# Optimization experiments

Measured on AMD Instinct MI355X. Metric: run time of the kernel, lower is better.

The kernel has to match this reference:

```python
import jax, jax.numpy as jnp
import numpy as np

D_WIN = 6
SIGMA = D_WIN / 2.0  # sigma = D/2
EPS = 1e-6


def _ln(x, g, b):
    m = jnp.mean(x, -1, keepdims=True)
    v = jnp.var(x, -1, keepdims=True)
    return (x - m) / jnp.sqrt(v + EPS) * g + b


def _cross_attn(q, kv, Wq, Wkv, Wproj, bproj, nh):
    # standard multi-head cross attention, no qkv bias (qkv_bias=False)
    B, S, C = q.shape
    N = kv.shape[1]
    hd = C // nh
    scale = hd ** -0.5
    qh = (q @ Wq).reshape(B, S, nh, hd).transpose(0, 2, 1, 3) * scale
    kvh = (kv @ Wkv).reshape(B, N, 2, nh, hd).transpose(2, 0, 3, 1, 4)
    k, v = kvh[0], kvh[1]
    attn = jax.nn.softmax(jnp.einsum('bhsd,bhnd->bhsn', qh, k), -1)
    x = jnp.einsum('bhsn,bhnd->bhsd', attn, v).transpose(0, 2, 1, 3).reshape(B, S, C)
    return x @ Wproj + bproj


def setup_inputs() -> dict:
    key = jax.random.key(0)
    ks = jax.random.split(key, 32)
    B, S, C, H, W = 32, 128, 384, 8, 512

    def lin(k, i, o):
        return jax.random.normal(k, (i, o), jnp.float32) * 0.02

    inp = {
        'q': jax.random.normal(ks[0], (B, S, C), jnp.float32),
        'kv': jax.random.normal(ks[1], (B, H * W, C), jnp.float32),
        # main attention linears (qkv_bias=False)
        'Wq': lin(ks[2], C, C),
        'Wkv': lin(ks[3], C, 2 * C),
        'Wproj': lin(ks[4], C, C), 'bproj': jnp.zeros((C,), jnp.float32),
        # position predictor
        'Wp_w': lin(ks[5], C, C), 'Wp_b': jnp.zeros((C,), jnp.float32),
        'vp_w': lin(ks[6], C, 1), 'vp_b': jnp.zeros((1,), jnp.float32),
        'Wqpos': lin(ks[7], C, C), 'bqpos': jnp.zeros((C,), jnp.float32),
        # simplified RCTC decoder projection
        'Wrctc': lin(ks[8], C, C), 'brctc': jnp.zeros((C,), jnp.float32),
        # pt_to_question cross attention (2 heads)
        'ca1_Wq': lin(ks[9], C, C), 'ca1_Wkv': lin(ks[10], C, 2 * C),
        'ca1_Wproj': lin(ks[11], C, C), 'ca1_bproj': jnp.zeros((C,), jnp.float32),
        # pt_to_image cross attention (2 heads)
        'ca2_Wq': lin(ks[12], C, C), 'ca2_Wkv': lin(ks[13], C, 2 * C),
        'ca2_Wproj': lin(ks[14], C, C), 'ca2_bproj': jnp.zeros((C,), jnp.float32),
        # layernorms
        'g_q1': jnp.ones((C,), jnp.float32), 'b_q1': jnp.zeros((C,), jnp.float32),
        'g_kv1': jnp.ones((C,), jnp.float32), 'b_kv1': jnp.zeros((C,), jnp.float32),
        'g_q2': jnp.ones((C,), jnp.float32), 'b_q2': jnp.zeros((C,), jnp.float32),
        'g_kv2': jnp.ones((C,), jnp.float32), 'b_kv2': jnp.zeros((C,), jnp.float32),
        'sz_h': H, 'sz_w': W,
    }
    return inp


def reference(q, kv, Wq, Wkv, Wproj, bproj, Wp_w, Wp_b, vp_w, vp_b, Wqpos, bqpos,
              Wrctc, brctc, ca1_Wq, ca1_Wkv, ca1_Wproj, ca1_bproj,
              ca2_Wq, ca2_Wkv, ca2_Wproj, ca2_bproj,
              g_q1, b_q1, g_kv1, b_kv1, g_q2, b_q2, g_kv2, b_kv2, sz_h, sz_w):
    B, N, C = kv.shape
    S = q.shape[1]
    H, W = sz_h, sz_w
    nh = 1
    hd = C // nh
    scale = hd ** -0.5

    # RCTC decoder (simplified): (B,N,C) -> (B,C,H,W) -> collapse H -> (B,W,C) -> linear
    kv_img = kv.transpose(0, 2, 1).reshape(B, C, H, W)
    dec = kv_img.mean(axis=2).transpose(0, 2, 1)  # (B, W, C)
    dec = dec @ Wrctc + brctc

    qh = (q @ Wq).reshape(B, S, nh, hd).transpose(0, 2, 1, 3) * scale  # (B,nh,S,hd)
    kvh = (dec @ Wkv).reshape(B, W, 2, nh, hd).transpose(2, 0, 3, 1, 4)
    k, v = kvh[0], kvh[1]  # (B,nh,W,hd)

    # position prediction branch
    p = q @ Wqpos + bqpos
    p = _cross_attn(_ln(p, g_q1, b_q1), _ln(q, g_kv1, b_kv1),
                    ca1_Wq, ca1_Wkv, ca1_Wproj, ca1_bproj, 2)
    p = _cross_attn(_ln(p, g_q2, b_q2), _ln(dec, g_kv2, b_kv2),
                    ca2_Wq, ca2_Wkv, ca2_Wproj, ca2_bproj, 2)
    p_t = jax.nn.sigmoid(jnp.tanh(p @ Wp_w + Wp_b) @ vp_w + vp_b) * W  # (B,S,1)

    # Gaussian window mask around predicted position
    idx = jnp.arange(W, dtype=jnp.float32)[None, None, None, :]     # (1,1,1,W)
    pexp = p_t[:, None, :, :]                                        # (B,1,S,1)
    gauss = jnp.exp(-(idx - pexp) ** 2 / (2.0 * SIGMA ** 2))         # (B,1,S,W)

    attn = jnp.einsum('bhsd,bhwd->bhsw', qh, k) * gauss
    attn = jax.nn.softmax(attn, -1)
    x = jnp.einsum('bhsw,bhwd->bhsd', attn, v).transpose(0, 2, 1, 3).reshape(B, S, C)
    return x @ Wproj + bproj
```

## Files before the change

kernel.cpp:

```cpp
#include <hip/hip_runtime.h>
#include <hip/hip_bf16.h>
#include <math.h>

#define B_ 32
#define S_ 128
#define C_ 384
#define H_ 8
#define W_ 512
#define NKV 4096

typedef __attribute__((ext_vector_type(8))) short short8;
typedef __attribute__((ext_vector_type(4))) float floatx4;

static __device__ __forceinline__ ushort f2bf(float v) {
    __hip_bfloat16 h = __float2bfloat16(v);
    return *(ushort*)&h;
}
static __device__ __forceinline__ float ldf(const float* p, size_t i) { return p[i]; }
static __device__ __forceinline__ float ldf(const ushort* p, size_t i) {
    union { uint u; float f; } c; c.u = (uint)p[i] << 16; return c.f;
}

static __device__ __forceinline__ void gl_lds16(const ushort* g, ushort* l) {
    __builtin_amdgcn_global_load_lds(
        (const __attribute__((address_space(1))) void*)g,
        (__attribute__((address_space(3))) void*)l, 16, 0, 0);
}

__global__ __launch_bounds__(256) void mean_kernel(const float* __restrict__ kv,
                                                   ushort* __restrict__ dec0b) {
    int v = blockIdx.x * blockDim.x + threadIdx.x;
    int total = B_ * W_ * (C_ / 4);
    if (v >= total) return;
    int c4  = v % (C_ / 4);
    int row = v / (C_ / 4);
    int b = row / W_;
    int w = row % W_;
    const float4* src = (const float4*)kv + (size_t)(b * NKV + w) * (C_ / 4) + c4;
    float4 s = {0.f, 0.f, 0.f, 0.f};
#pragma unroll
    for (int h = 0; h < H_; ++h) {
        float4 t = src[(size_t)h * W_ * (C_ / 4)];
        s.x += t.x; s.y += t.y; s.z += t.z; s.w += t.w;
    }
    ushort4 o;
    o.x = f2bf(s.x * 0.125f); o.y = f2bf(s.y * 0.125f);
    o.z = f2bf(s.z * 0.125f); o.w = f2bf(s.w * 0.125f);
    ((ushort4*)dec0b)[v] = o;
}

__global__ __launch_bounds__(256) void cast_kernel(const float* __restrict__ in,
                                                   ushort* __restrict__ out, int n4) {
    int v = blockIdx.x * blockDim.x + threadIdx.x;
    if (v >= n4) return;
    float4 f = ((const float4*)in)[v];
    ushort4 o;
    o.x = f2bf(f.x); o.y = f2bf(f.y); o.z = f2bf(f.z); o.w = f2bf(f.w);
    ((ushort4*)out)[v] = o;
}

struct WtDesc { const float* src[12]; ushort* dst[12]; int Kd[12]; int Nd[12]; };
__global__ __launch_bounds__(256) void wtcast_kernel(WtDesc d) {
    int wi = blockIdx.y;
    int idx = blockIdx.x * 256 + threadIdx.x;
    int K = d.Kd[wi], N = d.Nd[wi];
    if (idx >= K * N) return;
    int n = idx / K, k = idx % K;
    d.dst[wi][idx] = f2bf(d.src[wi][(size_t)k * N + n]);
}

__global__ __launch_bounds__(256) void bgemm_kernel(
    const ushort* __restrict__ A, const ushort* __restrict__ Bt,
    const float* __restrict__ bias, float* __restrict__ Cout,
    ushort* __restrict__ Cbf, int M, int N, int K, float alpha, int act)
{
    __shared__ ushort As[128 * 32];
    __shared__ ushort Bs[128 * 32];
    const int tid = threadIdx.x;
    const int bm = blockIdx.y * 128, bn = blockIdx.x * 128;
    const int wav = tid >> 6, lane = tid & 63;
    const int wm = (wav >> 1) * 64, wn = (wav & 1) * 64;
    const int lrow = lane & 15, lq = lane >> 4;

    floatx4 acc[4][4] = {};

    const int crow = tid >> 2, ccol = (tid & 3) * 8;
    const ushort* Ag0 = A + (size_t)(bm + crow) * K + ccol;
    const ushort* Ag1 = Ag0 + (size_t)64 * K;
    const ushort* Bg0 = Bt + (size_t)(bn + crow) * K + ccol;
    const ushort* Bg1 = Bg0 + (size_t)64 * K;
    ushort* AsP0 = &As[tid * 8];
    ushort* AsP1 = &As[2048 + tid * 8];
    ushort* BsP0 = &Bs[tid * 8];
    ushort* BsP1 = &Bs[2048 + tid * 8];

    for (int k0 = 0; k0 < K; k0 += 32) {
        gl_lds16(Ag0 + k0, AsP0);
        gl_lds16(Ag1 + k0, AsP1);
        gl_lds16(Bg0 + k0, BsP0);
        gl_lds16(Bg1 + k0, BsP1);
        __syncthreads();
        short8 af[4], bfr[4];
#pragma unroll
        for (int i = 0; i < 4; ++i)
            af[i] = *(const short8*)&As[(wm + 16 * i + lrow) * 32 + lq * 8];
#pragma unroll
        for (int j = 0; j < 4; ++j)
            bfr[j] = *(const short8*)&Bs[(wn + 16 * j + lrow) * 32 + lq * 8];
#pragma unroll
        for (int i = 0; i < 4; ++i)
#pragma unroll
            for (int j = 0; j < 4; ++j)
                acc[i][j] = __builtin_amdgcn_mfma_f32_16x16x32_bf16(af[i], bfr[j], acc[i][j], 0, 0, 0);
        __syncthreads();
    }

#pragma unroll
    for (int i = 0; i < 4; ++i)
#pragma unroll
        for (int j = 0; j < 4; ++j) {
            int row = bm + wm + 16 * i + lq * 4;
            int col = bn + wn + 16 * j + lrow;
            float bv = bias ? bias[col] : 0.f;
#pragma unroll
            for (int r = 0; r < 4; ++r) {
                float v = acc[i][j][r] * alpha + bv;
                if (act == 1) v = tanhf(v);
                size_t off = (size_t)(row + r) * N + col;
                if (Cout) Cout[off] = v;
                if (Cbf) Cbf[off] = f2bf(v);
            }
        }
}

static inline void bgemm(hipStream_t st, const ushort* A, const ushort* Bt,
                         const float* bias, float* Cout, ushort* Cbf,
                         int M, int N, int K, float alpha, int act) {
    dim3 grid(N / 128, M / 128), block(256);
    bgemm_kernel<<<grid, block, 0, st>>>(A, Bt, bias, Cout, Cbf, M, N, K, alpha, act);
}

struct BGArgs {
    const ushort* A; const ushort* Bt;
    const float* bias; float* outF; ushort* outB;
    int lda, ldb, ldo;
    long AsB, BsB, OsB;
    int AsH, BsH, OsH;
    int K, NH;
    float alpha; int act;
};
__global__ __launch_bounds__(256) void battn_kernel(BGArgs g) {
    __shared__ ushort As[128 * 40];
    __shared__ ushort Bs[64 * 40];
    const int bn = blockIdx.x * 64, bm = blockIdx.y * 128;
    const int bat = blockIdx.z, bb = bat / g.NH, hh = bat % g.NH;
    const ushort* A  = g.A  + (size_t)bb * g.AsB + (size_t)hh * g.AsH;
    const ushort* Bt = g.Bt + (size_t)bb * g.BsB + (size_t)hh * g.BsH;
    const int tid = threadIdx.x;
    const int wav = tid >> 6, lane = tid & 63;
    const int lrow = lane & 15, lq = lane >> 4;
    const int sr = tid >> 2, sc0 = (tid & 3) * 8;
    const ushort* Ag0 = A + (size_t)(bm + sr) * g.lda + sc0;
    const ushort* Ag1 = A + (size_t)(bm + sr + 64) * g.lda + sc0;
    const ushort* Bg  = Bt + (size_t)(bn + sr) * g.ldb + sc0;
    ushort* Asw0 = &As[sr * 40 + sc0];
    ushort* Asw1 = &As[(sr + 64) * 40 + sc0];
    ushort* Bsw  = &Bs[sr * 40 + sc0];

    floatx4 acc[2][4] = {};

    for (int k0 = 0; k0 < g.K; k0 += 32) {
        uint4 a0 = *(const uint4*)(Ag0 + k0);
        uint4 a1 = *(const uint4*)(Ag1 + k0);
        uint4 b  = *(const uint4*)(Bg + k0);
        __syncthreads();
        *(uint4*)Asw0 = a0; *(uint4*)Asw1 = a1; *(uint4*)Bsw = b;
        __syncthreads();
        short8 af0 = *(const short8*)&As[(wav * 32 + lrow) * 40 + lq * 8];
        short8 af1 = *(const short8*)&As[(wav * 32 + 16 + lrow) * 40 + lq * 8];
#pragma unroll
        for (int j = 0; j < 4; ++j) {
            short8 bf = *(const short8*)&Bs[(16 * j + lrow) * 40 + lq * 8];
            acc[0][j] = __builtin_amdgcn_mfma_f32_16x16x32_bf16(af0, bf, acc[0][j], 0, 0, 0);
            acc[1][j] = __builtin_amdgcn_mfma_f32_16x16x32_bf16(af1, bf, acc[1][j], 0, 0, 0);
        }
    }

#pragma unroll
    for (int i = 0; i < 2; ++i)
#pragma unroll
        for (int j = 0; j < 4; ++j) {
            int col = bn + 16 * j + lrow;
            float bv = g.bias ? g.bias[col] : 0.f;
            int row0 = bm + wav * 32 + 16 * i + lq * 4;
#pragma unroll
            for (int r = 0; r < 4; ++r) {
                float v = acc[i][j][r] * g.alpha + bv;
                if (g.act == 1) v = tanhf(v);
                size_t off = (size_t)bb * g.OsB + (size_t)hh * g.OsH
                           + (size_t)(row0 + r) * g.ldo + col;
                if (g.outF) g.outF[off] = v;
                if (g.outB) g.outB[off] = f2bf(v);
            }
        }
}

static inline void battn(hipStream_t st, const ushort* A, const ushort* Bt,
                         const float* bias, float* outF, ushort* outB,
                         int M, int N, int K, float alpha, int act,
                         int lda, long AsB, int AsH,
                         int ldb, long BsB, int BsH,
                         int ldo, long OsB, int OsH,
                         int NH, int nbat) {
    BGArgs g;
    g.A = A; g.Bt = Bt; g.bias = bias; g.outF = outF; g.outB = outB;
    g.lda = lda; g.ldb = ldb; g.ldo = ldo;
    g.AsB = AsB; g.BsB = BsB; g.OsB = OsB;
    g.AsH = AsH; g.BsH = BsH; g.OsH = OsH;
    g.K = K; g.NH = NH; g.alpha = alpha; g.act = act;
    dim3 grid(N / 64, M / 128, nbat);
    battn_kernel<<<grid, 256, 0, st>>>(g);
}

static inline void bgemm64(hipStream_t st, const ushort* A, const ushort* Bt,
                           const float* bias, float* outF, ushort* outB,
                           int M, int N, int K, float alpha, int act) {
    battn(st, A, Bt, bias, outF, outB, M, N, K, alpha, act,
          K, 0, 0, K, 0, 0, N, 0, 0, 1, 1);
}

template <typename T>
__global__ __launch_bounds__(128) void ln_kernel(const T* __restrict__ X,
    const float* __restrict__ g, const float* __restrict__ bb,
    ushort* __restrict__ Y) {
    int row = blockIdx.x;
    const T* x = X + (size_t)row * C_;
    ushort* y = Y + (size_t)row * C_;
    int t = threadIdx.x;
    float v0 = ldf(x, t), v1 = ldf(x, t + 128), v2 = ldf(x, t + 256);
    float s = v0 + v1 + v2, sq = v0 * v0 + v1 * v1 + v2 * v2;
    __shared__ float rs[128], rq[128];
    rs[t] = s; rq[t] = sq; __syncthreads();
    if (t < 64) {
        s = rs[t] + rs[t + 64]; sq = rq[t] + rq[t + 64];
        for (int o = 32; o; o >>= 1) { s += __shfl_down(s, o); sq += __shfl_down(sq, o); }
        if (t == 0) { rs[0] = s; rq[0] = sq; }
    }
    __syncthreads();
    float mean = rs[0] * (1.0f / C_);
    float var  = rq[0] * (1.0f / C_) - mean * mean;
    float inv  = rsqrtf(var + 1e-6f);
    y[t]       = f2bf((v0 - mean) * inv * g[t]       + bb[t]);
    y[t + 128] = f2bf((v1 - mean) * inv * g[t + 128] + bb[t + 128]);
    y[t + 256] = f2bf((v2 - mean) * inv * g[t + 256] + bb[t + 256]);
}

template <int NW, int GAUSS>
__global__ __launch_bounds__(256) void softmax_kernel(
    const float* __restrict__ sc, const float* __restrict__ ptv,
    ushort* __restrict__ P)
{
    int row = blockIdx.x * 4 + (threadIdx.x >> 6);
    int lane = threadIdx.x & 63;
    const float* s = sc + (size_t)row * NW;
    float pcen = GAUSS ? ptv[row] : 0.f;
    float vals[NW / 64];
    float m = -1e30f;
#pragma unroll
    for (int i = 0; i < NW / 64; ++i) {
        int w = lane + 64 * i;
        float v = s[w];
        if (GAUSS) { float dw = (float)w - pcen; v *= expf(dw * dw * (-1.0f / 18.0f)); }
        vals[i] = v; m = fmaxf(m, v);
    }
#pragma unroll
    for (int o = 32; o; o >>= 1) m = fmaxf(m, __shfl_xor(m, o));
    float sum = 0.f;
#pragma unroll
    for (int i = 0; i < NW / 64; ++i) { vals[i] = expf(vals[i] - m); sum += vals[i]; }
#pragma unroll
    for (int o = 32; o; o >>= 1) sum += __shfl_xor(sum, o);
    float rinv = 1.0f / sum;
    ushort* op = P + (size_t)row * NW;
#pragma unroll
    for (int i = 0; i < NW / 64; ++i) op[lane + 64 * i] = f2bf(vals[i] * rinv);
}

__global__ __launch_bounds__(256) void vtrans_kernel(
    const ushort* __restrict__ kvb, ushort* __restrict__ vt,
    int Nw, int C2, int CC)
{
    int b = blockIdx.z;
    int w0 = blockIdx.x * 32, c0 = blockIdx.y * 32;
    __shared__ ushort t[32][33];
    int tid = threadIdx.x;
    int wl = tid >> 3, c4 = (tid & 7) * 4;
    ushort4 v = *(const ushort4*)&kvb[((size_t)b * Nw + w0 + wl) * C2 + CC + c0 + c4];
    t[wl][c4] = v.x; t[wl][c4 + 1] = v.y; t[wl][c4 + 2] = v.z; t[wl][c4 + 3] = v.w;
    __syncthreads();
    int dl = tid >> 3, w4 = (tid & 7) * 4;
    ushort4 o;
    o.x = t[w4][dl]; o.y = t[w4 + 1][dl]; o.z = t[w4 + 2][dl]; o.w = t[w4 + 3][dl];
    *(ushort4*)&vt[((size_t)b * CC + c0 + dl) * Nw + w0 + w4] = o;
}

__global__ __launch_bounds__(128) void pt_kernel(const float* __restrict__ T,
    const float* __restrict__ vpw, const float* __restrict__ vpb,
    float* __restrict__ out) {
    int row = blockIdx.x;
    int t = threadIdx.x;
    const float* x = T + (size_t)row * C_;
    float s = x[t] * vpw[t] + x[t + 128] * vpw[t + 128] + x[t + 256] * vpw[t + 256];
    __shared__ float red[128];
    red[t] = s; __syncthreads();
    if (t < 64) {
        s = red[t] + red[t + 64];
        for (int o = 32; o; o >>= 1) s += __shfl_down(s, o);
        if (t == 0) {
            float z = s + vpb[0];
            out[row] = 512.0f / (1.0f + expf(-z));
        }
    }
}

extern "C" void kernel_launch(void* const* d_in, const int* in_sizes, int n_in,
                              void* d_out, int out_size, void* d_ws, size_t ws_size,
                              hipStream_t stream) {
    const float* q     = (const float*)d_in[0];
    const float* kv    = (const float*)d_in[1];
    const float* Wq    = (const float*)d_in[2];
    const float* Wkv   = (const float*)d_in[3];
    const float* Wproj = (const float*)d_in[4];
    const float* bproj = (const float*)d_in[5];
    const float* Wp_w  = (const float*)d_in[6];
    const float* Wp_b  = (const float*)d_in[7];
    const float* vp_w  = (const float*)d_in[8];
    const float* vp_b  = (const float*)d_in[9];
    const float* Wqpos = (const float*)d_in[10];
    const float* bqpos = (const float*)d_in[11];
    const float* Wrctc = (const float*)d_in[12];
    const float* brctc = (const float*)d_in[13];
    const float* ca1_Wq    = (const float*)d_in[14];
    const float* ca1_Wkv   = (const float*)d_in[15];
    const float* ca1_Wproj = (const float*)d_in[16];
    const float* ca1_bproj = (const float*)d_in[17];
    const float* ca2_Wq    = (const float*)d_in[18];
    const float* ca2_Wkv   = (const float*)d_in[19];
    const float* ca2_Wproj = (const float*)d_in[20];
    const float* ca2_bproj = (const float*)d_in[21];
    const float* g_q1  = (const float*)d_in[22];
    const float* b_q1  = (const float*)d_in[23];
    const float* g_kv1 = (const float*)d_in[24];
    const float* b_kv1 = (const float*)d_in[25];
    const float* g_q2  = (const float*)d_in[26];
    const float* b_q2  = (const float*)d_in[27];
    const float* g_kv2 = (const float*)d_in[28];
    const float* b_kv2 = (const float*)d_in[29];
    float* out = (float*)d_out;
    float* ws  = (float*)d_ws;

    ushort* dec0b = (ushort*)(ws);
    ushort* wb    = (ushort*)(ws + 3145728);
    ushort* qb    = (ushort*)(ws + 4251648);
    ushort* decb  = (ushort*)(ws + 5038080);
    ushort* qhb   = (ushort*)(ws + 8183808);
    float*  p     = ws + 8970240;
    ushort* pb    = (ushort*)(ws + 10543104);
    float*  t1    = ws + 11329536;
    ushort* t1b   = (ushort*)(ws + 12902400);
    ushort* t2b   = (ushort*)(ws + 13688832);
    ushort* qpb   = (ushort*)(ws + 16834560);
    ushort* kvb   = (ushort*)(ws + 17620992);
    ushort* vt    = (ushort*)(ws + 23912448);
    float*  sc    = ws + 27058176;
    ushort* Pb    = (ushort*)(ws + 31252480);
    ushort* xb    = (ushort*)(ws + 33349632);
    float*  ptb   = ws + 34136064;

    ushort* wbWq     = wb;
    ushort* wbWqpos  = wb + 147456;
    ushort* wbWrctc  = wb + 294912;
    ushort* wbC1Wq   = wb + 442368;
    ushort* wbC1Wp   = wb + 589824;
    ushort* wbC2Wq   = wb + 737280;
    ushort* wbC2Wp   = wb + 884736;
    ushort* wbWpw    = wb + 1032192;
    ushort* wbWproj  = wb + 1179648;
    ushort* wbWkv    = wb + 1327104;
    ushort* wbC1Wkv  = wb + 1622016;
    ushort* wbC2Wkv  = wb + 1916928;

    const float rs384 = 0.05103103630798288f;
    const float rs192 = 0.07216878364870323f;

    mean_kernel<<<(B_ * W_ * (C_ / 4) + 255) / 256, 256, 0, stream>>>(kv, dec0b);
    {
        WtDesc d;
        const float* s_[12] = {Wq, Wqpos, Wrctc, ca1_Wq, ca1_Wproj, ca2_Wq, ca2_Wproj,
                               Wp_w, Wproj, Wkv, ca1_Wkv, ca2_Wkv};
        ushort* t_[12] = {wbWq, wbWqpos, wbWrctc, wbC1Wq, wbC1Wp, wbC2Wq, wbC2Wp,
                          wbWpw, wbWproj, wbWkv, wbC1Wkv, wbC2Wkv};
        for (int i = 0; i < 12; ++i) {
            d.src[i] = s_[i]; d.dst[i] = t_[i];
            d.Kd[i] = 384; d.Nd[i] = (i >= 9) ? 768 : 384;
        }
        dim3 grid((294912 + 255) / 256, 12);
        wtcast_kernel<<<grid, 256, 0, stream>>>(d);
        cast_kernel<<<(393216 + 255) / 256, 256, 0, stream>>>(q, qb, 393216);
    }
    bgemm(stream, dec0b, wbWrctc, brctc, nullptr, decb, B_ * W_, 384, 384, 1.f, 0);
    bgemm64(stream, qb, wbWq, nullptr, nullptr, qhb, B_ * S_, 384, 384, rs384, 0);
    bgemm64(stream, qb, wbWqpos, bqpos, p, nullptr, B_ * S_, 384, 384, 1.f, 0);
    ln_kernel<float><<<B_ * S_, 128, 0, stream>>>(p, g_q1, b_q1, t1b);
    ln_kernel<float><<<B_ * S_, 128, 0, stream>>>(q, g_kv1, b_kv1, t2b);
    bgemm64(stream, t1b, wbC1Wq, nullptr, nullptr, qpb, B_ * S_, 384, 384, rs192, 0);
    bgemm64(stream, t2b, wbC1Wkv, nullptr, nullptr, kvb, B_ * S_, 768, 384, 1.f, 0);
    {
        dim3 gt(S_ / 32, C_ / 32, B_);
        vtrans_kernel<<<gt, 256, 0, stream>>>(kvb, vt, S_, 768, 384);
    }
    battn(stream, qpb, kvb, nullptr, sc, nullptr, 128, 128, 192, 1.f, 0,
          384, (long)S_ * 384, 192,
          768, (long)S_ * 768, 192,
          128, (long)2 * S_ * 128, S_ * 128, 2, 64);
    softmax_kernel<128, 0><<<(B_ * 2 * S_) / 4, 256, 0, stream>>>(sc, nullptr, Pb);
    battn(stream, Pb, vt, nullptr, nullptr, xb, 128, 192, 128, 1.f, 0,
          128, (long)2 * S_ * 128, S_ * 128,
          128, (long)C_ * S_, 192 * S_,
          384, (long)S_ * 384, 192, 2, 64);
    bgemm64(stream, xb, wbC1Wp, ca1_bproj, p, nullptr, B_ * S_, 384, 384, 1.f, 0);
    ln_kernel<float><<<B_ * S_, 128, 0, stream>>>(p, g_q2, b_q2, t1b);
    ln_kernel<ushort><<<B_ * W_, 128, 0, stream>>>(decb, g_kv2, b_kv2, t2b);
    bgemm64(stream, t1b, wbC2Wq, nullptr, nullptr, qpb, B_ * S_, 384, 384, rs192, 0);
    bgemm(stream, t2b, wbC2Wkv, nullptr, nullptr, kvb, B_ * W_, 768, 384, 1.f, 0);
    {
        dim3 gt(W_ / 32, C_ / 32, B_);
        vtrans_kernel<<<gt, 256, 0, stream>>>(kvb, vt, W_, 768, 384);
    }
    battn(stream, qpb, kvb, nullptr, sc, nullptr, 128, 512, 192, 1.f, 0,
          384, (long)S_ * 384, 192,
          768, (long)W_ * 768, 192,
          512, (long)2 * S_ * 512, S_ * 512, 2, 64);
    softmax_kernel<512, 0><<<(B_ * 2 * S_) / 4, 256, 0, stream>>>(sc, nullptr, Pb);
    battn(stream, Pb, vt, nullptr, nullptr, xb, 128, 192, 512, 1.f, 0,
          512, (long)2 * S_ * 512, S_ * 512,
          512, (long)C_ * W_, 192 * W_,
          384, (long)S_ * 384, 192, 2, 64);
    bgemm64(stream, xb, wbC2Wp, ca2_bproj, p, pb, B_ * S_, 384, 384, 1.f, 0);
    bgemm64(stream, pb, wbWpw, Wp_b, t1, nullptr, B_ * S_, 384, 384, 1.f, 1);
    pt_kernel<<<B_ * S_, 128, 0, stream>>>(t1, vp_w, vp_b, ptb);
    bgemm(stream, decb, wbWkv, nullptr, nullptr, kvb, B_ * W_, 768, 384, 1.f, 0);
    {
        dim3 gt(W_ / 32, C_ / 32, B_);
        vtrans_kernel<<<gt, 256, 0, stream>>>(kvb, vt, W_, 768, 384);
    }
    battn(stream, qhb, kvb, nullptr, sc, nullptr, 128, 512, 384, 1.f, 0,
          384, (long)S_ * 384, 0,
          768, (long)W_ * 768, 0,
          512, (long)S_ * 512, 0, 1, 32);
    softmax_kernel<512, 1><<<(B_ * S_) / 4, 256, 0, stream>>>(sc, ptb, Pb);
    battn(stream, Pb, vt, nullptr, nullptr, xb, 128, 384, 512, 1.f, 0,
          512, (long)S_ * 512, 0,
          512, (long)C_ * W_, 0,
          384, (long)S_ * 384, 0, 1, 32);
    bgemm64(stream, xb, wbWproj, bproj, out, nullptr, B_ * S_, 384, 384, 1.f, 0);
}
```

Baseline: 639.8 us.

## Batch independent GEMMs and layernorms into grouped launches, retile attention GEMM

Independent GEMMs are grouped into a single multi-job launch indexed by blockIdx.z, and pairs of layernorms are merged into one kernel, cutting launch count and letting small GEMMs fill the GPU alongside larger ones. The weight cast/transpose now goes through an LDS tile with vectorized loads and stores instead of strided scalar reads. The GEMM kernel drops global_load_lds in favour of register-staged loads into padded LDS with a double barrier, and the batched attention GEMM moves from 128x64 to 64x64 tiles for more blocks. Risks include idle early-exit blocks in the grouped grids and losing the direct-to-LDS load path.

```diff
diff --git a/kernel.cpp b/kernel.cpp
--- a/kernel.cpp
+++ b/kernel.cpp
@@ -19,12 +19,6 @@
 static __device__ __forceinline__ float ldf(const float* p, size_t i) { return p[i]; }
 static __device__ __forceinline__ float ldf(const ushort* p, size_t i) {
     union { uint u; float f; } c; c.u = (uint)p[i] << 16; return c.f;
-}
-
-static __device__ __forceinline__ void gl_lds16(const ushort* g, ushort* l) {
-    __builtin_amdgcn_global_load_lds(
-        (const __attribute__((address_space(1))) void*)g,
-        (__attribute__((address_space(3))) void*)l, 16, 0, 0);
 }
 
 __global__ __launch_bounds__(256) void mean_kernel(const float* __restrict__ kv,
@@ -62,57 +56,71 @@
 struct WtDesc { const float* src[12]; ushort* dst[12]; int Kd[12]; int Nd[12]; };
 __global__ __launch_bounds__(256) void wtcast_kernel(WtDesc d) {
     int wi = blockIdx.y;
-    int idx = blockIdx.x * 256 + threadIdx.x;
     int K = d.Kd[wi], N = d.Nd[wi];
-    if (idx >= K * N) return;
-    int n = idx / K, k = idx % K;
-    d.dst[wi][idx] = f2bf(d.src[wi][(size_t)k * N + n]);
-}
-
-__global__ __launch_bounds__(256) void bgemm_kernel(
-    const ushort* __restrict__ A, const ushort* __restrict__ Bt,
-    const float* __restrict__ bias, float* __restrict__ Cout,
-    ushort* __restrict__ Cbf, int M, int N, int K, float alpha, int act)
-{
-    __shared__ ushort As[128 * 32];
-    __shared__ ushort Bs[128 * 32];
+    int tiles_n = N / 32;
+    int tile = blockIdx.x;
+    if (tile >= (K / 32) * tiles_n) return;
+    int k0 = (tile / tiles_n) * 32, n0 = (tile % tiles_n) * 32;
+    __shared__ float t[32][33];
+    int tid = threadIdx.x;
+    int r = tid >> 3, c4 = (tid & 7) * 4;
+    float4 v = *(const float4*)&d.src[wi][(size_t)(k0 + r) * N + n0 + c4];
+    t[r][c4] = v.x; t[r][c4 + 1] = v.y; t[r][c4 + 2] = v.z; t[r][c4 + 3] = v.w;
+    __syncthreads();
+    int c = tid >> 3, k4 = (tid & 7) * 4;
+    ushort4 o;
+    o.x = f2bf(t[k4][c]); o.y = f2bf(t[k4 + 1][c]);
+    o.z = f2bf(t[k4 + 2][c]); o.w = f2bf(t[k4 + 3][c]);
+    *(ushort4*)&d.dst[wi][(size_t)(n0 + c) * K + k0 + k4] = o;
+}
+
+struct GJob {
+    const ushort* A; const ushort* Bt;
+    const float* bias; float* Cout; ushort* Cbf;
+    int M, N, K; float alpha; int act;
+};
+struct GJobs { GJob j[3]; };
+
+__global__ __launch_bounds__(256) void bgemm_kernel(GJobs gs) {
+    const GJob g = gs.j[blockIdx.z];
+    const int bm = blockIdx.y * 128, bn = blockIdx.x * 128;
+    if (bm >= g.M || bn >= g.N) return;
+    __shared__ ushort As[128 * 40];
+    __shared__ ushort Bs[128 * 40];
     const int tid = threadIdx.x;
-    const int bm = blockIdx.y * 128, bn = blockIdx.x * 128;
     const int wav = tid >> 6, lane = tid & 63;
     const int wm = (wav >> 1) * 64, wn = (wav & 1) * 64;
     const int lrow = lane & 15, lq = lane >> 4;
 
     floatx4 acc[4][4] = {};
 
-    const int crow = tid >> 2, ccol = (tid & 3) * 8;
-    const ushort* Ag0 = A + (size_t)(bm + crow) * K + ccol;
-    const ushort* Ag1 = Ag0 + (size_t)64 * K;
-    const ushort* Bg0 = Bt + (size_t)(bn + crow) * K + ccol;
-    const ushort* Bg1 = Bg0 + (size_t)64 * K;
-    ushort* AsP0 = &As[tid * 8];
-    ushort* AsP1 = &As[2048 + tid * 8];
-    ushort* BsP0 = &Bs[tid * 8];
-    ushort* BsP1 = &Bs[2048 + tid * 8];
-
-    for (int k0 = 0; k0 < K; k0 += 32) {
-        gl_lds16(Ag0 + k0, AsP0);
-        gl_lds16(Ag1 + k0, AsP1);
-        gl_lds16(Bg0 + k0, BsP0);
-        gl_lds16(Bg1 + k0, BsP1);
+    const int sr = tid >> 1, sc0 = (tid & 1) * 16;
+    const ushort* Ag = g.A + (size_t)(bm + sr) * g.K + sc0;
+    const ushort* Bg = g.Bt + (size_t)(bn + sr) * g.K + sc0;
+    ushort* Asw = &As[sr * 40 + sc0];
+    ushort* Bsw = &Bs[sr * 40 + sc0];
+
+    for (int k0 = 0; k0 < g.K; k0 += 32) {
+        uint4 a0 = *(const uint4*)(Ag + k0);
+        uint4 a1 = *(const uint4*)(Ag + k0 + 8);
+        uint4 b0 = *(const uint4*)(Bg + k0);
+        uint4 b1 = *(const uint4*)(Bg + k0 + 8);
+        __syncthreads();
+        *(uint4*)Asw = a0; *(uint4*)(Asw + 8) = a1;
+        *(uint4*)Bsw = b0; *(uint4*)(Bsw + 8) = b1;
         __syncthreads();
         short8 af[4], bfr[4];
 #pragma unroll
         for (int i = 0; i < 4; ++i)
-            af[i] = *(const short8*)&As[(wm + 16 * i + lrow) * 32 + lq * 8];
+            af[i] = *(const short8*)&As[(wm + 16 * i + lrow) * 40 + lq * 8];
 #pragma unroll
         for (int j = 0; j < 4; ++j)
-            bfr[j] = *(const short8*)&Bs[(wn + 16 * j + lrow) * 32 + lq * 8];
+            bfr[j] = *(const short8*)&Bs[(wn + 16 * j + lrow) * 40 + lq * 8];
 #pragma unroll
         for (int i = 0; i < 4; ++i)
 #pragma unroll
             for (int j = 0; j < 4; ++j)
                 acc[i][j] = __builtin_amdgcn_mfma_f32_16x16x32_bf16(af[i], bfr[j], acc[i][j], 0, 0, 0);
-        __syncthreads();
     }
 
 #pragma unroll
@@ -121,23 +129,29 @@
         for (int j = 0; j < 4; ++j) {
             int row = bm + wm + 16 * i + lq * 4;
             int col = bn + wn + 16 * j + lrow;
-            float bv = bias ? bias[col] : 0.f;
+            float bv = g.bias ? g.bias[col] : 0.f;
 #pragma unroll
             for (int r = 0; r < 4; ++r) {
-                float v = acc[i][j][r] * alpha + bv;
-                if (act == 1) v = tanhf(v);
-                size_t off = (size_t)(row + r) * N + col;
-                if (Cout) Cout[off] = v;
-                if (Cbf) Cbf[off] = f2bf(v);
+                float v = acc[i][j][r] * g.alpha + bv;
+                if (g.act == 1) v = tanhf(v);
+                size_t off = (size_t)(row + r) * g.N + col;
+                if (g.Cout) g.Cout[off] = v;
+                if (g.Cbf) g.Cbf[off] = f2bf(v);
             }
         }
 }
 
-static inline void bgemm(hipStream_t st, const ushort* A, const ushort* Bt,
-                         const float* bias, float* Cout, ushort* Cbf,
-                         int M, int N, int K, float alpha, int act) {
-    dim3 grid(N / 128, M / 128), block(256);
-    bgemm_kernel<<<grid, block, 0, st>>>(A, Bt, bias, Cout, Cbf, M, N, K, alpha, act);
+static inline void bgemmJ(hipStream_t st, int nj, const GJob* js) {
+    GJobs gs;
+    int mx = 0, my = 0;
+    for (int i = 0; i < nj; ++i) {
+        gs.j[i] = js[i];
+        int nx = js[i].N / 128, ny = js[i].M / 128;
+        if (nx > mx) mx = nx;
+        if (ny > my) my = ny;
+    }
+    for (int i = nj; i < 3; ++i) gs.j[i] = js[0];
+    bgemm_kernel<<<dim3(mx, my, nj), 256, 0, st>>>(gs);
 }
 
 struct BGArgs {
@@ -150,9 +164,9 @@
     float alpha; int act;
 };
 __global__ __launch_bounds__(256) void battn_kernel(BGArgs g) {
-    __shared__ ushort As[128 * 40];
+    __shared__ ushort As[64 * 40];
     __shared__ ushort Bs[64 * 40];
-    const int bn = blockIdx.x * 64, bm = blockIdx.y * 128;
+    const int bn = blockIdx.x * 64, bm = blockIdx.y * 64;
     const int bat = blockIdx.z, bb = bat / g.NH, hh = bat % g.NH;
     const ushort* A  = g.A  + (size_t)bb * g.AsB + (size_t)hh * g.AsH;
     const ushort* Bt = g.Bt + (size_t)bb * g.BsB + (size_t)hh * g.BsH;
@@ -160,49 +174,42 @@
     const int wav = tid >> 6, lane = tid & 63;
     const int lrow = lane & 15, lq = lane >> 4;
     const int sr = tid >> 2, sc0 = (tid & 3) * 8;
-    const ushort* Ag0 = A + (size_t)(bm + sr) * g.lda + sc0;
-    const ushort* Ag1 = A + (size_t)(bm + sr + 64) * g.lda + sc0;
-    const ushort* Bg  = Bt + (size_t)(bn + sr) * g.ldb + sc0;
-    ushort* Asw0 = &As[sr * 40 + sc0];
-    ushort* Asw1 = &As[(sr + 64) * 40 + sc0];
-    ushort* Bsw  = &Bs[sr * 40 + sc0];
-
-    floatx4 acc[2][4] = {};
+    const ushort* Ag = A  + (size_t)(bm + sr) * g.lda + sc0;
+    const ushort* Bg = Bt + (size_t)(bn + sr) * g.ldb + sc0;
+    ushort* Asw = &As[sr * 40 + sc0];
+    ushort* Bsw = &Bs[sr * 40 + sc0];
+
+    floatx4 acc[4] = {};
 
     for (int k0 = 0; k0 < g.K; k0 += 32) {
-        uint4 a0 = *(const uint4*)(Ag0 + k0);
-        uint4 a1 = *(const uint4*)(Ag1 + k0);
-        uint4 b  = *(const uint4*)(Bg + k0);
+        uint4 a = *(const uint4*)(Ag + k0);
+        uint4 b = *(const uint4*)(Bg + k0);
         __syncthreads();
-        *(uint4*)Asw0 = a0; *(uint4*)Asw1 = a1; *(uint4*)Bsw = b;
+        *(uint4*)Asw = a; *(uint4*)Bsw = b;
         __syncthreads();
-        short8 af0 = *(const short8*)&As[(wav * 32 + lrow) * 40 + lq * 8];
-        short8 af1 = *(const short8*)&As[(wav * 32 + 16 + lrow) * 40 + lq * 8];
+        short8 af = *(const short8*)&As[(wav * 16 + lrow) * 40 + lq * 8];
 #pragma unroll
         for (int j = 0; j < 4; ++j) {
             short8 bf = *(const short8*)&Bs[(16 * j + lrow) * 40 + lq * 8];
-            acc[0][j] = __builtin_amdgcn_mfma_f32_16x16x32_bf16(af0, bf, acc[0][j], 0, 0, 0);
-            acc[1][j] = __builtin_amdgcn_mfma_f32_16x16x32_bf16(af1, bf, acc[1][j], 0, 0, 0);
+            acc[j] = __builtin_amdgcn_mfma_f32_16x16x32_bf16(af, bf, acc[j], 0, 0, 0);
         }
     }
 
 #pragma unroll
-    for (int i = 0; i < 2; ++i)
-#pragma unroll
-        for (int j = 0; j < 4; ++j) {
-            int col = bn + 16 * j + lrow;
-            float bv = g.bias ? g.bias[col] : 0.f;
-            int row0 = bm + wav * 32 + 16 * i + lq * 4;
-#pragma unroll
-            for (int r = 0; r < 4; ++r) {
-                float v = acc[i][j][r] * g.alpha + bv;
-                if (g.act == 1) v = tanhf(v);
-                size_t off = (size_t)bb * g.OsB + (size_t)hh * g.OsH
-                           + (size_t)(row0 + r) * g.ldo + col;
-                if (g.outF) g.outF[off] = v;
-                if (g.outB) g.outB[off] = f2bf(v);
-            }
+    for (int j = 0; j < 4; ++j) {
+        int col = bn + 16 * j + lrow;
+        float bv = g.bias ? g.bias[col] : 0.f;
+        int row0 = bm + wav * 16 + lq * 4;
+#pragma unroll
+        for (int r = 0; r < 4; ++r) {
+            float v = acc[j][r] * g.alpha + bv;
+            if (g.act == 1) v = tanhf(v);
+            size_t off = (size_t)bb * g.OsB + (size_t)hh * g.OsH
+                       + (size_t)(row0 + r) * g.ldo + col;
+            if (g.outF) g.outF[off] = v;
+            if (g.outB) g.outB[off] = f2bf(v);
         }
+    }
 }
 
 static inline void battn(hipStream_t st, const ushort* A, const ushort* Bt,
@@ -218,7 +225,7 @@
     g.AsB = AsB; g.BsB = BsB; g.OsB = OsB;
     g.AsH = AsH; g.BsH = BsH; g.OsH = OsH;
     g.K = K; g.NH = NH; g.alpha = alpha; g.act = act;
-    dim3 grid(N / 64, M / 128, nbat);
+    dim3 grid(N / 64, M / 64, nbat);
     battn_kernel<<<grid, 256, 0, st>>>(g);
 }
 
@@ -229,15 +236,22 @@
           K, 0, 0, K, 0, 0, N, 0, 0, 1, 1);
 }
 
-template <typename T>
-__global__ __launch_bounds__(128) void ln_kernel(const T* __restrict__ X,
-    const float* __restrict__ g, const float* __restrict__ bb,
-    ushort* __restrict__ Y) {
+struct Ln2Desc {
+    const void* X0; const float* g0; const float* b0; ushort* Y0; int bf0; int rows0;
+    const void* X1; const float* g1; const float* b1; ushort* Y1; int bf1;
+};
+__global__ __launch_bounds__(128) void ln2_kernel(Ln2Desc d) {
     int row = blockIdx.x;
-    const T* x = X + (size_t)row * C_;
+    const void* X; const float* g; const float* bb; ushort* Y; int isbf;
+    if (row < d.rows0) { X = d.X0; g = d.g0; bb = d.b0; Y = d.Y0; isbf = d.bf0; }
+    else { row -= d.rows0; X = d.X1; g = d.g1; bb = d.b1; Y = d.Y1; isbf = d.bf1; }
+    const float*  xf = (const float*)X + (size_t)row * C_;
+    const ushort* xb = (const ushort*)X + (size_t)row * C_;
     ushort* y = Y + (size_t)row * C_;
     int t = threadIdx.x;
-    float v0 = ldf(x, t), v1 = ldf(x, t + 128), v2 = ldf(x, t + 256);
+    float v0, v1, v2;
+    if (isbf) { v0 = ldf(xb, t); v1 = ldf(xb, t + 128); v2 = ldf(xb, t + 256); }
+    else      { v0 = ldf(xf, t); v1 = ldf(xf, t + 128); v2 = ldf(xf, t + 256); }
     float s = v0 + v1 + v2, sq = v0 * v0 + v1 * v1 + v2 * v2;
     __shared__ float rs[128], rq[128];
     rs[t] = s; rq[t] = sq; __syncthreads();
@@ -404,17 +418,29 @@
             d.src[i] = s_[i]; d.dst[i] = t_[i];
             d.Kd[i] = 384; d.Nd[i] = (i >= 9) ? 768 : 384;
         }
-        dim3 grid((294912 + 255) / 256, 12);
+        dim3 grid(288, 12);
         wtcast_kernel<<<grid, 256, 0, stream>>>(d);
         cast_kernel<<<(393216 + 255) / 256, 256, 0, stream>>>(q, qb, 393216);
     }
-    bgemm(stream, dec0b, wbWrctc, brctc, nullptr, decb, B_ * W_, 384, 384, 1.f, 0);
-    bgemm64(stream, qb, wbWq, nullptr, nullptr, qhb, B_ * S_, 384, 384, rs384, 0);
-    bgemm64(stream, qb, wbWqpos, bqpos, p, nullptr, B_ * S_, 384, 384, 1.f, 0);
-    ln_kernel<float><<<B_ * S_, 128, 0, stream>>>(p, g_q1, b_q1, t1b);
-    ln_kernel<float><<<B_ * S_, 128, 0, stream>>>(q, g_kv1, b_kv1, t2b);
-    bgemm64(stream, t1b, wbC1Wq, nullptr, nullptr, qpb, B_ * S_, 384, 384, rs192, 0);
-    bgemm64(stream, t2b, wbC1Wkv, nullptr, nullptr, kvb, B_ * S_, 768, 384, 1.f, 0);
+    {
+        GJob js[3];
+        js[0] = {dec0b, wbWrctc, brctc, nullptr, decb, B_ * W_, 384, 384, 1.f, 0};
+        js[1] = {qb, wbWq, nullptr, nullptr, qhb, B_ * S_, 384, 384, rs384, 0};
+        js[2] = {qb, wbWqpos, bqpos, p, nullptr, B_ * S_, 384, 384, 1.f, 0};
+        bgemmJ(stream, 3, js);
+    }
+    {
+        Ln2Desc d;
+        d.X0 = p; d.g0 = g_q1;  d.b0 = b_q1;  d.Y0 = t1b; d.bf0 = 0; d.rows0 = B_ * S_;
+        d.X1 = q; d.g1 = g_kv1; d.b1 = b_kv1; d.Y1 = t2b; d.bf1 = 0;
+        ln2_kernel<<<2 * B_ * S_, 128, 0, stream>>>(d);
+    }
+    {
+        GJob js[2];
+        js[0] = {t1b, wbC1Wq, nullptr, nullptr, qpb, B_ * S_, 384, 384, rs192, 0};
+        js[1] = {t2b, wbC1Wkv, nullptr, nullptr, kvb, B_ * S_, 768, 384, 1.f, 0};
+        bgemmJ(stream, 2, js);
+    }
     {
         dim3 gt(S_ / 32, C_ / 32, B_);
         vtrans_kernel<<<gt, 256, 0, stream>>>(kvb, vt, S_, 768, 384);
@@ -429,10 +455,18 @@
           128, (long)C_ * S_, 192 * S_,
           384, (long)S_ * 384, 192, 2, 64);
     bgemm64(stream, xb, wbC1Wp, ca1_bproj, p, nullptr, B_ * S_, 384, 384, 1.f, 0);
-    ln_kernel<float><<<B_ * S_, 128, 0, stream>>>(p, g_q2, b_q2, t1b);
-    ln_kernel<ushort><<<B_ * W_, 128, 0, stream>>>(decb, g_kv2, b_kv2, t2b);
-    bgemm64(stream, t1b, wbC2Wq, nullptr, nullptr, qpb, B_ * S_, 384, 384, rs192, 0);
-    bgemm(stream, t2b, wbC2Wkv, nullptr, nullptr, kvb, B_ * W_, 768, 384, 1.f, 0);
+    {
+        Ln2Desc d;
+        d.X0 = p;    d.g0 = g_q2;  d.b0 = b_q2;  d.Y0 = t1b; d.bf0 = 0; d.rows0 = B_ * S_;
+        d.X1 = decb; d.g1 = g_kv2; d.b1 = b_kv2; d.Y1 = t2b; d.bf1 = 1;
+        ln2_kernel<<<B_ * S_ + B_ * W_, 128, 0, stream>>>(d);
+    }
+    {
+        GJob js[2];
+        js[0] = {t1b, wbC2Wq, nullptr, nullptr, qpb, B_ * S_, 384, 384, rs192, 0};
+        js[1] = {t2b, wbC2Wkv, nullptr, nullptr, kvb, B_ * W_, 768, 384, 1.f, 0};
+        bgemmJ(stream, 2, js);
+    }
     {
         dim3 gt(W_ / 32, C_ / 32, B_);
         vtrans_kernel<<<gt, 256, 0, stream>>>(kvb, vt, W_, 768, 384);
@@ -447,9 +481,13 @@
           512, (long)C_ * W_, 192 * W_,
           384, (long)S_ * 384, 192, 2, 64);
     bgemm64(stream, xb, wbC2Wp, ca2_bproj, p, pb, B_ * S_, 384, 384, 1.f, 0);
-    bgemm64(stream, pb, wbWpw, Wp_b, t1, nullptr, B_ * S_, 384, 384, 1.f, 1);
+    {
+        GJob js[2];
+        js[0] = {pb, wbWpw, Wp_b, t1, nullptr, B_ * S_, 384, 384, 1.f, 1};
+        js[1] = {decb, wbWkv, nullptr, nullptr, kvb, B_ * W_, 768, 384, 1.f, 0};
+        bgemmJ(stream, 2, js);
+    }
     pt_kernel<<<B_ * S_, 128, 0, stream>>>(t1, vp_w, vp_b, ptb);
-    bgemm(stream, decb, wbWkv, nullptr, nullptr, kvb, B_ * W_, 768, 384, 1.f, 0);
     {
         dim3 gt(W_ / 32, C_ / 32, B_);
         vtrans_kernel<<<gt, 256, 0, stream>>>(kvb, vt, W_, 768, 384);
```

Result: faster. 586.7 us (-8.3%).
